# Performance work log

Hardware: AMD Instinct MI355X
Metric: run time of the kernel (lower is better)

## Reference

```python
import jax, jax.numpy as jnp
import numpy as np

NUM_HEADS = 8
WINDOW = 3
LOCAL_LEN = WINDOW * WINDOW
SR_RATIO = 8


def _normalize(v, eps=1e-12):
    n = jnp.linalg.norm(v, axis=-1, keepdims=True)
    return v / jnp.maximum(n, eps)


def _layernorm(v, g, b, eps=1e-5):
    m = v.mean(-1, keepdims=True)
    var = ((v - m) ** 2).mean(-1, keepdims=True)
    return (v - m) / jnp.sqrt(var + eps) * g + b


def _unfold3(x, H, W):
    # x: [B, C, H, W] -> [B, C, 9, H*W]  (kernel 3, pad 1, stride 1; torch nn.Unfold layout)
    B, C = x.shape[0], x.shape[1]
    xp = jnp.pad(x, ((0, 0), (0, 0), (1, 1), (1, 1)))
    patches = jnp.stack([xp[:, :, di:di + H, dj:dj + W]
                         for di in range(WINDOW) for dj in range(WINDOW)], axis=2)
    return patches.reshape(B, C, LOCAL_LEN, H * W)


def _forward(x, relative_coords_table, seq_length_scale, q_w, q_b, kv_w, kv_b,
             temperature, query_embedding, sr_w, sr_b, norm_g, norm_b,
             cpb_fc1_w, cpb_fc1_b, cpb_fc2_w, cpb_fc2_b,
             rel_bias_local, learnable_tokens, learnable_bias,
             proj_w, proj_b, relative_pos_index, padding_mask, H, W):
    B, N, C = x.shape
    hd = C // NUM_HEADS
    pool_H, pool_W = H // SR_RATIO, W // SR_RATIO
    pool_len = pool_H * pool_W

    # ---- queries ----
    q = (x @ q_w.T + q_b).reshape(B, N, NUM_HEADS, hd).transpose(0, 2, 1, 3)  # [B,h,N,d]
    q_norm = _normalize(q)
    q_scaled = (q_norm + query_embedding) * jax.nn.softplus(temperature) * seq_length_scale

    # ---- local k/v via unfold ----
    kv = x @ kv_w.T + kv_b  # [B,N,2C]
    k_loc = _normalize(kv[..., :C].reshape(B, N, NUM_HEADS, hd)).reshape(B, N, C)
    kv_img = jnp.concatenate([k_loc, kv[..., C:]], -1).transpose(0, 2, 1).reshape(B, 2 * C, H, W)
    kv_unf = _unfold3(kv_img, H, W).reshape(B, 2 * NUM_HEADS, hd, LOCAL_LEN, N)
    kv_unf = kv_unf.transpose(0, 1, 4, 2, 3)  # [B,2h,N,d,9]
    k_local, v_local = kv_unf[:, :NUM_HEADS], kv_unf[:, NUM_HEADS:]

    attn_local = jnp.einsum('bhnd,bhndl->bhnl', q_scaled, k_local) + rel_bias_local[:, None, :]
    attn_local = jnp.where(padding_mask, -jnp.inf, attn_local)

    # ---- pooled global k/v ----
    x_img = x.transpose(0, 2, 1).reshape(B, C, H, W)
    x_sr = jax.nn.gelu(jnp.einsum('oc,bchw->bohw', sr_w, x_img) + sr_b[None, :, None, None],
                       approximate=False)
    x_pool = x_sr.reshape(B, C, pool_H, SR_RATIO, pool_W, SR_RATIO).mean((3, 5))
    x_pool = x_pool.reshape(B, C, pool_len).transpose(0, 2, 1)
    x_pool = _layernorm(x_pool, norm_g, norm_b)
    kv_p = (x_pool @ kv_w.T + kv_b).reshape(B, pool_len, 2 * NUM_HEADS, hd).transpose(0, 2, 1, 3)
    k_pool, v_pool = kv_p[:, :NUM_HEADS], kv_p[:, NUM_HEADS:]

    # ---- continuous relative position bias (extrapolation path) ----
    cpb = jax.nn.relu(relative_coords_table @ cpb_fc1_w.T + cpb_fc1_b) @ cpb_fc2_w.T + cpb_fc2_b  # [T,h]
    pool_bias = cpb[relative_pos_index].reshape(N, pool_len, NUM_HEADS).transpose(2, 0, 1)  # [h,N,P]

    attn_pool = jnp.einsum('bhnd,bhpd->bhnp', q_scaled, _normalize(k_pool)) + pool_bias

    attn = jax.nn.softmax(jnp.concatenate([attn_local, attn_pool], -1), axis=-1)
    a_loc, a_pool = attn[..., :LOCAL_LEN], attn[..., LOCAL_LEN:]

    lt = jnp.einsum('bhnd,hdl->bhnl', q_norm, learnable_tokens) + learnable_bias + a_loc
    x_local = jnp.einsum('bhnl,bhndl->bhnd', lt, v_local)
    x_p = jnp.einsum('bhnp,bhpd->bhnd', a_pool, v_pool)
    out = (x_local + x_p).transpose(0, 2, 1, 3).reshape(B, N, C)
    return out @ proj_w.T + proj_b


def setup_inputs() -> dict:
    key = jax.random.key(0)
    B, H, W, C = 4, 64, 64, 256
    N = H * W
    hd = C // NUM_HEADS
    pool_H, pool_W = H // SR_RATIO, W // SR_RATIO
    pool_len = pool_H * pool_W

    # padding mask + per-query valid window length (get_seqlen_and_mask)
    ii, jj = np.meshgrid(np.arange(H), np.arange(W), indexing='ij')
    cols = []
    for di in range(WINDOW):
        for dj in range(WINDOW):
            ni, nj = ii + di - 1, jj + dj - 1
            cols.append(((ni < 0) | (ni >= H) | (nj < 0) | (nj >= W)).reshape(-1))
    padding_mask = np.stack(cols, -1)  # [N, 9], True = outside image
    local_len = (~padding_mask).sum(-1, keepdims=True).astype(np.float32)
    seq_length_scale = np.log(local_len + pool_len)  # [N, 1]

    # get_relative_position_cpb((H,W), (pool_H,pool_W))
    axis_q = np.arange(H, dtype=np.float64)
    axis_k = axis_q.reshape(pool_H, SR_RATIO).mean(-1)
    kh, kw = np.meshgrid(axis_k, axis_k, indexing='ij')
    qh, qw = np.meshgrid(axis_q, axis_q, indexing='ij')
    rel_h = (qh.ravel()[:, None] - kh.ravel()[None, :]) / (H - 1) * 8
    rel_w = (qw.ravel()[:, None] - kw.ravel()[None, :]) / (W - 1) * 8
    rel = np.stack([rel_h, rel_w], -1).reshape(-1, 2)
    table, idx = np.unique(rel, axis=0, return_inverse=True)
    table = np.sign(table) * np.log2(np.abs(table) + 1.0) / np.log2(8.0)

    ks = jax.random.split(key, 12)

    def nrm(k, shape, std=0.02):
        return jax.random.normal(k, shape, jnp.float32) * std

    return {
        'x': jax.random.normal(ks[0], (B, N, C), jnp.float32),
        'relative_coords_table': jnp.asarray(table, jnp.float32),
        'seq_length_scale': jnp.asarray(seq_length_scale, jnp.float32),
        'q_w': nrm(ks[1], (C, C)), 'q_b': jnp.zeros((C,), jnp.float32),
        'kv_w': nrm(ks[2], (2 * C, C)), 'kv_b': jnp.zeros((2 * C,), jnp.float32),
        'temperature': jnp.full((NUM_HEADS, 1, 1), float(np.log(np.expm1(1.0 / 0.24))), jnp.float32),
        'query_embedding': nrm(ks[3], (NUM_HEADS, 1, hd)),
        'sr_w': nrm(ks[4], (C, C)), 'sr_b': jnp.zeros((C,), jnp.float32),
        'norm_g': jnp.ones((C,), jnp.float32), 'norm_b': jnp.zeros((C,), jnp.float32),
        'cpb_fc1_w': nrm(ks[5], (512, 2), 0.1), 'cpb_fc1_b': jnp.zeros((512,), jnp.float32),
        'cpb_fc2_w': nrm(ks[6], (NUM_HEADS, 512)), 'cpb_fc2_b': jnp.zeros((NUM_HEADS,), jnp.float32),
        'rel_bias_local': nrm(ks[7], (NUM_HEADS, LOCAL_LEN), 0.0004),
        'learnable_tokens': nrm(ks[8], (NUM_HEADS, hd, LOCAL_LEN)),
        'learnable_bias': jnp.zeros((NUM_HEADS, 1, LOCAL_LEN), jnp.float32),
        'proj_w': nrm(ks[9], (C, C)), 'proj_b': jnp.zeros((C,), jnp.float32),
        'relative_pos_index': jnp.asarray(idx, jnp.int32),
        'padding_mask': jnp.asarray(padding_mask),
        'H': H, 'W': W,
    }


def reference(x, relative_coords_table, seq_length_scale, q_w, q_b, kv_w, kv_b,
              temperature, query_embedding, sr_w, sr_b, norm_g, norm_b,
              cpb_fc1_w, cpb_fc1_b, cpb_fc2_w, cpb_fc2_b,
              rel_bias_local, learnable_tokens, learnable_bias,
              proj_w, proj_b, relative_pos_index, padding_mask, H, W):
    return _forward(x, relative_coords_table, seq_length_scale, q_w, q_b, kv_w, kv_b,
                    temperature, query_embedding, sr_w, sr_b, norm_g, norm_b,
                    cpb_fc1_w, cpb_fc1_b, cpb_fc2_w, cpb_fc2_b,
                    rel_bias_local, learnable_tokens, learnable_bias,
                    proj_w, proj_b, relative_pos_index, padding_mask, H, W)
```

## Files before the change

kernel.cpp:

```cpp
#include <hip/hip_runtime.h>
#include <math.h>


typedef unsigned short ushort_t;
typedef __attribute__((ext_vector_type(8))) _Float16 half8;
typedef __attribute__((ext_vector_type(2))) _Float16 half2_t;
typedef __attribute__((ext_vector_type(4))) float f32x4;

static __device__ __forceinline__ ushort_t f2h(float f) {
    _Float16 h = (_Float16)f;
    return *(ushort_t*)&h;
}

static __device__ __forceinline__ float fdot2f(half2_t a, half2_t b, float c) {
#if __has_builtin(__builtin_amdgcn_fdot2)
    return __builtin_amdgcn_fdot2(a, b, c, false);
#else
    return (float)a[0] * (float)b[0] + (float)a[1] * (float)b[1] + c;
#endif
}

template <int CTRL>
static __device__ __forceinline__ float dpp_addf(float x) {
    int v = __builtin_amdgcn_update_dpp(
        0, __builtin_bit_cast(int, x), CTRL, 0xF, 0xF, true);
    return x + __builtin_bit_cast(float, v);
}
static __device__ __forceinline__ float quad_sumf(float x) {
    return dpp_addf<0x4E>(dpp_addf<0xB1>(x));
}
static __device__ __forceinline__ float sum16f(float x) {
    return dpp_addf<0x128>(dpp_addf<0x124>(quad_sumf(x)));
}

#define GLOAD16(g, l)                                                        \
    __builtin_amdgcn_global_load_lds(                                        \
        (const __attribute__((address_space(1))) unsigned int*)(g),          \
        (__attribute__((address_space(3))) unsigned int*)(l), 16, 0, 0)

template <int TM, int TN>
__global__ __launch_bounds__(256) void mfma_hgemm(
    const ushort_t* __restrict__ Ag, const ushort_t* __restrict__ Bg,
    const float* __restrict__ bias, float* __restrict__ out0,
    ushort_t* __restrict__ qh_out, ushort_t* __restrict__ kvh,
    ushort_t* __restrict__ xsrh, int mode)
{
    const int K = 256;
    const int IM = TM / 32;
    const int JN = TN / 32;
    __shared__ ushort_t Ah[2][TM * 32];
    __shared__ ushort_t Bh[2][TN * 32];

    const int t = threadIdx.x;
    const int w = t >> 6;
    const int lane = t & 63;
    const int bm = blockIdx.y * TM;
    const int bn = blockIdx.x * TN;
    const int wm = (w >> 1) * (TM / 2);
    const int wn = (w & 1) * (TN / 2);

    f32x4 acc[IM][JN];
#pragma unroll
    for (int i = 0; i < IM; ++i)
#pragma unroll
        for (int j = 0; j < JN; ++j) acc[i][j] = f32x4{0.f, 0.f, 0.f, 0.f};

    const int lrow  = t >> 2;
    const int lk8sw = ((t & 3) ^ ((t >> 3) & 3)) * 8;

#define STAGE(bufi, k0s)                                                     \
    do {                                                                     \
        _Pragma("unroll")                                                    \
        for (int r = 0; r < TM / 64; ++r)                                    \
            GLOAD16(Ag + (size_t)(bm + r * 64 + lrow) * K + (k0s) + lk8sw,   \
                    &Ah[bufi][(unsigned)(r * 64 + w * 16) * 32]);            \
        _Pragma("unroll")                                                    \
        for (int r = 0; r < TN / 64; ++r)                                    \
            GLOAD16(Bg + (size_t)(bn + r * 64 + lrow) * K + (k0s) + lk8sw,   \
                    &Bh[bufi][(unsigned)(r * 64 + w * 16) * 32]);            \
    } while (0)

    const int fr   = lane & 15;
    const int sws8 = ((lane >> 4) ^ ((fr >> 1) & 3)) * 8;

    STAGE(0, 0);
    __syncthreads();
    int buf = 0;
    for (int k0 = 0; k0 < K; k0 += 32) {
        if (k0 + 32 < K) STAGE(buf ^ 1, k0 + 32);

        half8 af[IM], bf[JN];
#pragma unroll
        for (int i = 0; i < IM; ++i)
            af[i] = *(const half8*)&Ah[buf][(unsigned)(wm + i * 16 + fr) * 32 + sws8];
#pragma unroll
        for (int j = 0; j < JN; ++j)
            bf[j] = *(const half8*)&Bh[buf][(unsigned)(wn + j * 16 + fr) * 32 + sws8];
#pragma unroll
        for (int i = 0; i < IM; ++i)
#pragma unroll
            for (int j = 0; j < JN; ++j)
                acc[i][j] = __builtin_amdgcn_mfma_f32_16x16x32_f16(af[i], bf[j], acc[i][j], 0, 0, 0);

        __syncthreads();
        buf ^= 1;
    }
#undef STAGE

    const int q4 = (lane >> 4) * 4;
#pragma unroll
    for (int i = 0; i < IM; ++i) {
#pragma unroll
        for (int jp = 0; jp < JN / 2; ++jp) {
#pragma unroll
            for (int r = 0; r < 4; ++r) {
                const int row = bm + wm + i * 16 + q4 + r;
                const int col0 = bn + wn + jp * 32 + fr;
                const int col1 = col0 + 16;
                float v0 = acc[i][2 * jp][r] + bias[col0];
                float v1 = acc[i][2 * jp + 1][r] + bias[col1];
                if (mode == 0) {
                    if (col0 < 256) {
                        qh_out[(size_t)row * 256 + col0] = f2h(v0);
                        qh_out[(size_t)row * 256 + col1] = f2h(v1);
                    } else if (col0 < 512) {
                        const float ss = sum16f(v0 * v0 + v1 * v1);
                        const float invn = 1.0f / fmaxf(sqrtf(ss), 1e-12f);
                        kvh[(size_t)row * 512 + (col0 - 256)] = f2h(v0 * invn);
                        kvh[(size_t)row * 512 + (col1 - 256)] = f2h(v1 * invn);
                    } else if (col0 < 768) {
                        kvh[(size_t)row * 512 + (col0 - 256)] = f2h(v0);
                        kvh[(size_t)row * 512 + (col1 - 256)] = f2h(v1);
                    } else {
                        v0 = 0.5f * v0 * (1.0f + erff(v0 * 0.70710678118654752f));
                        v1 = 0.5f * v1 * (1.0f + erff(v1 * 0.70710678118654752f));
                        xsrh[(size_t)row * 256 + (col0 - 768)] = f2h(v0);
                        xsrh[(size_t)row * 256 + (col1 - 768)] = f2h(v1);
                    }
                } else if (mode == 2) {
                    if (col0 < 256) {
                        const float ss = sum16f(v0 * v0 + v1 * v1);
                        const float invn = 1.0f / fmaxf(sqrtf(ss), 1e-12f);
                        v0 *= invn; v1 *= invn;
                    }
                    kvh[(size_t)row * 512 + col0] = f2h(v0);
                    kvh[(size_t)row * 512 + col1] = f2h(v1);
                } else {
                    out0[(size_t)row * 256 + col0] = v0;
                    out0[(size_t)row * 256 + col1] = v1;
                }
            }
        }
    }
}

__global__ __launch_bounds__(256) void prep_cpb(
    const float4* __restrict__ x, ushort4* __restrict__ xh, int n4, int nprep,
    const float* __restrict__ qw, const float* __restrict__ kvw,
    const float* __restrict__ srw, const float* __restrict__ pw,
    const float* __restrict__ qb, const float* __restrict__ kvb,
    const float* __restrict__ srb,
    ushort_t* __restrict__ Wall, ushort_t* __restrict__ Pw,
    float* __restrict__ ball,
    const float* __restrict__ table, const float* __restrict__ w1,
    const float* __restrict__ b1, const float* __restrict__ w2,
    const float* __restrict__ b2, float* __restrict__ outc, int T)
{
    if (blockIdx.x >= nprep) {
        const int wv = threadIdx.x >> 6;
        const int lane = threadIdx.x & 63;
        const int row = (blockIdx.x - nprep) * 4 + wv;
        if (row >= T) return;
        const float t0 = table[(size_t)row * 2];
        const float t1 = table[(size_t)row * 2 + 1];
        const int base = lane * 8;

        const float4* w1p = (const float4*)(w1 + (size_t)base * 2);
        float4 wa = w1p[0], wb = w1p[1], wc = w1p[2], wd = w1p[3];
        float4 ba = *(const float4*)(b1 + base);
        float4 bb = *(const float4*)(b1 + base + 4);
        float h[8];
        h[0] = fmaxf(fmaf(t1, wa.y, fmaf(t0, wa.x, ba.x)), 0.f);
        h[1] = fmaxf(fmaf(t1, wa.w, fmaf(t0, wa.z, ba.y)), 0.f);
        h[2] = fmaxf(fmaf(t1, wb.y, fmaf(t0, wb.x, ba.z)), 0.f);
        h[3] = fmaxf(fmaf(t1, wb.w, fmaf(t0, wb.z, ba.w)), 0.f);
        h[4] = fmaxf(fmaf(t1, wc.y, fmaf(t0, wc.x, bb.x)), 0.f);
        h[5] = fmaxf(fmaf(t1, wc.w, fmaf(t0, wc.z, bb.y)), 0.f);
        h[6] = fmaxf(fmaf(t1, wd.y, fmaf(t0, wd.x, bb.z)), 0.f);
        h[7] = fmaxf(fmaf(t1, wd.w, fmaf(t0, wd.z, bb.w)), 0.f);

#pragma unroll
        for (int hh = 0; hh < 8; ++hh) {
            const float4* w2p = (const float4*)(w2 + (size_t)hh * 512 + base);
            float4 p0 = w2p[0], p1 = w2p[1];
            float s = h[0]*p0.x + h[1]*p0.y + h[2]*p0.z + h[3]*p0.w
                    + h[4]*p1.x + h[5]*p1.y + h[6]*p1.z + h[7]*p1.w;
#pragma unroll
            for (int off = 1; off <= 32; off <<= 1) s += __shfl_xor(s, off);
            if (lane == 0) outc[(size_t)row * 8 + hh] = s + b2[hh];
        }
        return;
    }

    int idx = blockIdx.x * 256 + threadIdx.x;
    if (idx < n4) {
        float4 v = x[idx];
        ushort4 h;
        h.x = f2h(v.x); h.y = f2h(v.y); h.z = f2h(v.z); h.w = f2h(v.w);
        xh[idx] = h;
    }
    if (idx < 262144) {
        int nn = idx >> 8, k = idx & 255;
        float a;
        if (nn < 256)      a = qw[nn * 256 + k];
        else if (nn < 768) a = kvw[(nn - 256) * 256 + k];
        else               a = srw[(nn - 768) * 256 + k];
        Wall[idx] = f2h(a);
    }
    if (idx < 65536) Pw[idx] = f2h(pw[idx]);
    if (idx < 1024) {
        float bv;
        if (idx < 256)      bv = qb[idx];
        else if (idx < 768) bv = kvb[idx - 256];
        else                bv = srb[idx - 768];
        ball[idx] = bv;
    }
}

__global__ __launch_bounds__(256) void pool_ln(
    const ushort_t* __restrict__ xsr, const float* __restrict__ g,
    const float* __restrict__ be, ushort_t* __restrict__ xpool, int Hh, int Ww)
{
    const int C = 256;
    const int Nn = Hh * Ww;
    int b = blockIdx.x >> 6;
    int pidx = blockIdx.x & 63;
    int ph = pidx >> 3, pw = pidx & 7;
    int tid = threadIdx.x;
    float s = 0.f;
    for (int si = 0; si < 8; ++si) {
        int i = ph * 8 + si;
        const ushort_t* rowp = xsr + ((size_t)b * Nn + (size_t)i * Ww + pw * 8) * C + tid;
#pragma unroll
        for (int sj = 0; sj < 8; ++sj)
            s += (float)(*(const _Float16*)&rowp[(size_t)sj * C]);
    }
    s *= (1.f / 64.f);
    __shared__ float red[256];
    red[tid] = s; __syncthreads();
    for (int st = 128; st; st >>= 1) { if (tid < st) red[tid] += red[tid + st]; __syncthreads(); }
    float mean = red[0] * (1.f / 256.f);
    __syncthreads();
    float dv = s - mean;
    red[tid] = dv * dv; __syncthreads();
    for (int st = 128; st; st >>= 1) { if (tid < st) red[tid] += red[tid + st]; __syncthreads(); }
    float var = red[0] * (1.f / 256.f);
    xpool[(size_t)blockIdx.x * C + tid] = f2h(dv * rsqrtf(var + 1e-5f) * g[tid] + be[tid]);
}

__global__ __launch_bounds__(256) void attn_v8(
    const ushort_t* __restrict__ qh_g,
    const ushort_t* __restrict__ kvh,
    const ushort_t* __restrict__ kvph,
    const int* __restrict__ rpi,
    const float* __restrict__ cpbB,
    const float* __restrict__ sls, const float* __restrict__ temp,
    const float* __restrict__ qe, const float* __restrict__ rbl,
    const float* __restrict__ ltok, const float* __restrict__ lbias,
    ushort_t* __restrict__ attno_hf)
{
    const int h = blockIdx.y, b = blockIdx.z;
    const int t = threadIdx.x;
    const int i = blockIdx.x;

    __shared__ half8 kp_s[64][4];
    __shared__ half8 vp_s[64][4];
    __shared__ ushort_t pb_s[64][66];
    __shared__ float lts[9][32];
    __shared__ float rbl_s[9], lb_s[9], qe_s[32];

    {
        const int p = t >> 2;
        const int g4s = t & 3;
        const ushort_t* gk = kvph + ((size_t)(b * 64 + p)) * 512 + h * 32 + g4s * 8;
        kp_s[p][g4s] = *(const half8*)gk;
        vp_s[p][g4s] = *(const half8*)(gk + 256);
        const int rbase = i * 4096;
        for (int u = t; u < 4096; u += 256) {
            const int idx = rpi[rbase + u];
            pb_s[u >> 6][u & 63] = f2h(cpbB[(size_t)idx * 8 + h]);
        }
        for (int u = t; u < 288; u += 256) lts[u % 9][u / 9] = ltok[h * 288 + u];
        if (t < 9)  { rbl_s[t] = rbl[h * 9 + t]; lb_s[t] = lbias[h * 9 + t]; }
        if (t >= 64 && t < 96) qe_s[t - 64] = qe[h * 32 + (t - 64)];
    }
    __syncthreads();

    const int w = t >> 6;
    const int lane = t & 63;
    const int qi = lane >> 2;
    const int g4 = lane & 3;
    const int co = g4 * 8;
    const int j = w * 16 + qi;
    const int n = i * 64 + j;
    const size_t gq = (size_t)b * 4096 + n;

    const float tm = temp[h];
    const float sp = (tm > 20.f) ? tm : log1pf(expf(tm));

    float qv[8];
    {
        const half8 q8 = *(const half8*)(qh_g + gq * 256 + h * 32 + co);
        float ss = 0.f;
#pragma unroll
        for (int d = 0; d < 8; ++d) { qv[d] = (float)q8[d]; ss += qv[d] * qv[d]; }
        ss = quad_sumf(ss);
        const float invn = 1.0f / fmaxf(sqrtf(ss), 1e-12f);
#pragma unroll
        for (int d = 0; d < 8; ++d) qv[d] *= invn;
    }

    float lt[9];
#pragma unroll
    for (int l = 0; l < 9; ++l) {
        float dl = 0.f;
        const float4* lw = (const float4*)&lts[l][co];
#pragma unroll
        for (int c4 = 0; c4 < 2; ++c4) {
            float4 w4 = lw[c4];
            dl += qv[4*c4+0]*w4.x + qv[4*c4+1]*w4.y + qv[4*c4+2]*w4.z + qv[4*c4+3]*w4.w;
        }
        dl = quad_sumf(dl);
        lt[l] = dl + lb_s[l];
    }

    const float scal = sp * sls[n];
    half2_t qh[4];
#pragma unroll
    for (int c = 0; c < 4; ++c) {
        float a = (qv[2*c+0] + qe_s[co + 2*c+0]) * scal;
        float bq = (qv[2*c+1] + qe_s[co + 2*c+1]) * scal;
        qh[c] = half2_t{(_Float16)a, (_Float16)bq};
    }

    float sl[9];
#pragma unroll
    for (int l = 0; l < 9; ++l) {
        const int di = l / 3 - 1, dj = l % 3 - 1;
        const int ii = i + di;
        const int jn = j + dj;
        const bool ok = (ii >= 0) && (ii < 64) && (jn >= 0) && (jn < 64);
        const int ic = max(min(ii, 63), 0);
        const int jc = max(min(jn, 63), 0);
        const half8 k8 = *(const half8*)(kvh + ((size_t)(b * 4096 + ic * 64 + jc)) * 512 + h * 32 + co);
        float dk = 0.f;
        dk = fdot2f(qh[0], __builtin_shufflevector(k8, k8, 0, 1), dk);
        dk = fdot2f(qh[1], __builtin_shufflevector(k8, k8, 2, 3), dk);
        dk = fdot2f(qh[2], __builtin_shufflevector(k8, k8, 4, 5), dk);
        dk = fdot2f(qh[3], __builtin_shufflevector(k8, k8, 6, 7), dk);
        dk = quad_sumf(dk);
        sl[l] = ok ? (dk + rbl_s[l]) : -INFINITY;
    }

    float m = sl[0];
#pragma unroll
    for (int l = 1; l < 9; ++l) m = fmaxf(m, sl[l]);

    half2_t oh[4];
#pragma unroll
    for (int c = 0; c < 4; ++c) oh[c] = half2_t{(_Float16)0.f, (_Float16)0.f};
    float Z = 0.f;

    for (int cch = 0; cch < 8; ++cch) {
        float s8[8];
        float pbv[8];
#pragma unroll
        for (int c = 0; c < 4; ++c) {
            const half2_t p2 = *(const half2_t*)&pb_s[j][cch * 8 + 2 * c];
            pbv[2*c]   = (float)p2[0];
            pbv[2*c+1] = (float)p2[1];
        }
#pragma unroll
        for (int k = 0; k < 8; ++k) {
            const int p = cch * 8 + k;
            const half8 k8 = kp_s[p][g4];
            float acc = 0.f;
            acc = fdot2f(qh[0], __builtin_shufflevector(k8, k8, 0, 1), acc);
            acc = fdot2f(qh[1], __builtin_shufflevector(k8, k8, 2, 3), acc);
            acc = fdot2f(qh[2], __builtin_shufflevector(k8, k8, 4, 5), acc);
            acc = fdot2f(qh[3], __builtin_shufflevector(k8, k8, 6, 7), acc);
            acc = quad_sumf(acc);
            s8[k] = acc + pbv[k];
        }
        float cmax = s8[0];
#pragma unroll
        for (int k = 1; k < 8; ++k) cmax = fmaxf(cmax, s8[k]);
        const float m_new = fmaxf(m, cmax);
        const float factor = __expf(m - m_new);
        Z *= factor;
        const _Float16 fh = (_Float16)factor;
        const half2_t f2 = half2_t{fh, fh};
#pragma unroll
        for (int c = 0; c < 4; ++c) oh[c] *= f2;
        m = m_new;
#pragma unroll
        for (int k = 0; k < 8; ++k) {
            const float a = __expf(s8[k] - m);
            Z += a;
            const _Float16 ah = (_Float16)a;
            const half2_t a2 = half2_t{ah, ah};
            const half8 v8 = vp_s[cch * 8 + k][g4];
            oh[0] = a2 * __builtin_shufflevector(v8, v8, 0, 1) + oh[0];
            oh[1] = a2 * __builtin_shufflevector(v8, v8, 2, 3) + oh[1];
            oh[2] = a2 * __builtin_shufflevector(v8, v8, 4, 5) + oh[2];
            oh[3] = a2 * __builtin_shufflevector(v8, v8, 6, 7) + oh[3];
        }
    }

#pragma unroll
    for (int l = 0; l < 9; ++l) { sl[l] = __expf(sl[l] - m); Z += sl[l]; }

#pragma unroll
    for (int l = 0; l < 9; ++l) {
        const int di = l / 3 - 1, dj = l % 3 - 1;
        const int ii = i + di;
        const int jn = j + dj;
        const bool ok = (ii >= 0) && (ii < 64) && (jn >= 0) && (jn < 64);
        const int ic = max(min(ii, 63), 0);
        const int jc = max(min(jn, 63), 0);
        const float coef = ok ? (sl[l] + lt[l] * Z) : 0.f;
        const half8 v8 = *(const half8*)(kvh + ((size_t)(b * 4096 + ic * 64 + jc)) * 512 + 256 + h * 32 + co);
        const _Float16 ch = (_Float16)coef;
        const half2_t c2 = half2_t{ch, ch};
        oh[0] = c2 * __builtin_shufflevector(v8, v8, 0, 1) + oh[0];
        oh[1] = c2 * __builtin_shufflevector(v8, v8, 2, 3) + oh[1];
        oh[2] = c2 * __builtin_shufflevector(v8, v8, 4, 5) + oh[2];
        oh[3] = c2 * __builtin_shufflevector(v8, v8, 6, 7) + oh[3];
    }

    const float invZ = 1.0f / Z;
    ushort4* outp = (ushort4*)(attno_hf + gq * 256 + h * 32 + co);
#pragma unroll
    for (int c4 = 0; c4 < 2; ++c4) {
        ushort4 u;
        u.x = f2h((float)oh[2*c4+0][0] * invZ);
        u.y = f2h((float)oh[2*c4+0][1] * invZ);
        u.z = f2h((float)oh[2*c4+1][0] * invZ);
        u.w = f2h((float)oh[2*c4+1][1] * invZ);
        outp[c4] = u;
    }
}

extern "C" void kernel_launch(void* const* d_in, const int* in_sizes, int n_in,
                              void* d_out, int out_size, void* d_ws, size_t ws_size,
                              hipStream_t stream)
{
    const float* x    = (const float*)d_in[0];
    const float* tbl  = (const float*)d_in[1];
    const float* sls  = (const float*)d_in[2];
    const float* q_w  = (const float*)d_in[3];
    const float* q_b  = (const float*)d_in[4];
    const float* kv_w = (const float*)d_in[5];
    const float* kv_b = (const float*)d_in[6];
    const float* temp = (const float*)d_in[7];
    const float* qe   = (const float*)d_in[8];
    const float* sr_w = (const float*)d_in[9];
    const float* sr_b = (const float*)d_in[10];
    const float* ng   = (const float*)d_in[11];
    const float* nb   = (const float*)d_in[12];
    const float* f1w  = (const float*)d_in[13];
    const float* f1b  = (const float*)d_in[14];
    const float* f2w  = (const float*)d_in[15];
    const float* f2b  = (const float*)d_in[16];
    const float* rbl  = (const float*)d_in[17];
    const float* ltok = (const float*)d_in[18];
    const float* lbias= (const float*)d_in[19];
    const float* pw   = (const float*)d_in[20];
    const float* pb   = (const float*)d_in[21];
    const int*   rpi  = (const int*)d_in[22];

    const int C = 256, Hh = 64, Ww = 64, Nn = Hh * Ww;
    const int B = in_sizes[0] / (Nn * C);
    const int T = in_sizes[1] / 2;
    const int M = B * Nn;

    float* ws = (float*)d_ws;
    size_t o = 0;
    ushort_t* qh    = (ushort_t*)(ws + o); o += (size_t)M * C / 2;
    ushort_t* kvh   = (ushort_t*)(ws + o); o += (size_t)M * C;
    ushort_t* xsrh  = (ushort_t*)(ws + o); o += (size_t)M * C / 2;
    ushort_t* xpoolh= (ushort_t*)(ws + o); o += (size_t)B * 64 * C / 2;
    ushort_t* kvph  = (ushort_t*)(ws + o); o += (size_t)B * 64 * C;
    float* cpbB  = ws + o; o += (size_t)T * 8;
    ushort_t* xh   = (ushort_t*)(ws + o); o += (size_t)M * C / 2;
    ushort_t* Wall = (ushort_t*)(ws + o); o += 1024 * 256 / 2;
    ushort_t* Pwh  = (ushort_t*)(ws + o); o += 256 * 256 / 2;
    float* ball = ws + o; o += 1024;
    ushort_t* attno_hf = xh;

    dim3 blk(256);
    const int n4x = M * C / 4;
    const int nprep = (n4x + 255) / 256;
    const int ncpb  = (T + 3) / 4;

    prep_cpb<<<nprep + ncpb, blk, 0, stream>>>(
        (const float4*)x, (ushort4*)xh, n4x,
        nprep, q_w, kv_w, sr_w, pw, q_b, kv_b, sr_b, Wall, Pwh, ball,
        tbl, f1w, f1b, f2w, f2b, cpbB, T);
    mfma_hgemm<128, 128><<<dim3(8, M / 128), blk, 0, stream>>>(
        xh, Wall, ball, nullptr, qh, kvh, xsrh, 0);
    pool_ln<<<B * 64, blk, 0, stream>>>(xsrh, ng, nb, xpoolh, Hh, Ww);
    mfma_hgemm<64, 64><<<dim3(8, (B * 64) / 64), blk, 0, stream>>>(
        xpoolh, Wall + 256 * 256, ball + 256, nullptr, nullptr, kvph, nullptr, 2);
    attn_v8<<<dim3(64, 8, B), blk, 0, stream>>>(
        qh, kvh, kvph, rpi, cpbB, sls, temp, qe, rbl, ltok, lbias, attno_hf);
    mfma_hgemm<64, 64><<<dim3(4, M / 64), blk, 0, stream>>>(
        attno_hf, Pwh, pb, (float*)d_out, nullptr, nullptr, nullptr, 1);
}
```

Measured before the change: 229.1 us.

## Pipeline GEMM loads with vmcnt waits, XCD-aware block remap, and narrower tiles

Restructures the fp16 MFMA GEMM main loop so that two stages are prefetched up front. Each step waits on a partial vmcnt count and a raw s_barrier instead of a full __syncthreads, letting global-to-LDS loads overlap compute. It raises wave priority around the MFMA block and remaps workgroup IDs so consecutive tiles land on the same XCD for L2 locality. The input projection GEMM switches to 128x64 tiles with twice as many blocks. The risks are subtle ordering hazards in the manual waitcnt/barrier scheme and a remap that assumes the block count is a multiple of 8.

After: 208.0 us. 9.2% less time.

```diff
diff --git a/kernel.cpp b/kernel.cpp
--- a/kernel.cpp
+++ b/kernel.cpp
@@ -48,14 +48,20 @@
     const int K = 256;
     const int IM = TM / 32;
     const int JN = TN / 32;
+    constexpr int LPS = TM / 64 + TN / 64;
     __shared__ ushort_t Ah[2][TM * 32];
     __shared__ ushort_t Bh[2][TN * 32];
 
     const int t = threadIdx.x;
     const int w = t >> 6;
     const int lane = t & 63;
-    const int bm = blockIdx.y * TM;
-    const int bn = blockIdx.x * TN;
+
+    const int nwg = gridDim.x * gridDim.y;
+    int wg = blockIdx.y * gridDim.x + blockIdx.x;
+    wg = (wg & 7) * (nwg >> 3) + (wg >> 3);
+    const int bm = (wg / gridDim.x) * TM;
+    const int bn = (wg % gridDim.x) * TN;
+
     const int wm = (w >> 1) * (TM / 2);
     const int wn = (w & 1) * (TN / 2);
 
@@ -83,28 +89,45 @@
     const int fr   = lane & 15;
     const int sws8 = ((lane >> 4) ^ ((fr >> 1) & 3)) * 8;
 
+#define COMPUTE(bufi)                                                        \
+    do {                                                                     \
+        half8 af[IM], bf[JN];                                                \
+        _Pragma("unroll")                                                    \
+        for (int i2 = 0; i2 < IM; ++i2)                                      \
+            af[i2] = *(const half8*)&Ah[bufi][(unsigned)(wm + i2 * 16 + fr) * 32 + sws8]; \
+        _Pragma("unroll")                                                    \
+        for (int j2 = 0; j2 < JN; ++j2)                                      \
+            bf[j2] = *(const half8*)&Bh[bufi][(unsigned)(wn + j2 * 16 + fr) * 32 + sws8]; \
+        __builtin_amdgcn_s_setprio(1);                                       \
+        _Pragma("unroll")                                                    \
+        for (int i2 = 0; i2 < IM; ++i2)                                      \
+            _Pragma("unroll")                                                \
+            for (int j2 = 0; j2 < JN; ++j2)                                  \
+                acc[i2][j2] = __builtin_amdgcn_mfma_f32_16x16x32_f16(        \
+                    af[i2], bf[j2], acc[i2][j2], 0, 0, 0);                   \
+        __builtin_amdgcn_s_setprio(0);                                       \
+    } while (0)
+
     STAGE(0, 0);
-    __syncthreads();
+    STAGE(1, 32);
     int buf = 0;
-    for (int k0 = 0; k0 < K; k0 += 32) {
-        if (k0 + 32 < K) STAGE(buf ^ 1, k0 + 32);
-
-        half8 af[IM], bf[JN];
-#pragma unroll
-        for (int i = 0; i < IM; ++i)
-            af[i] = *(const half8*)&Ah[buf][(unsigned)(wm + i * 16 + fr) * 32 + sws8];
-#pragma unroll
-        for (int j = 0; j < JN; ++j)
-            bf[j] = *(const half8*)&Bh[buf][(unsigned)(wn + j * 16 + fr) * 32 + sws8];
-#pragma unroll
-        for (int i = 0; i < IM; ++i)
-#pragma unroll
-            for (int j = 0; j < JN; ++j)
-                acc[i][j] = __builtin_amdgcn_mfma_f32_16x16x32_f16(af[i], bf[j], acc[i][j], 0, 0, 0);
-
-        __syncthreads();
+#pragma unroll
+    for (int s = 0; s < K / 32 - 1; ++s) {
+        asm volatile("s_waitcnt vmcnt(%0)" :: "n"(LPS) : "memory");
+        __builtin_amdgcn_s_barrier();
+        asm volatile("" ::: "memory");
+        COMPUTE(buf);
+        asm volatile("" ::: "memory");
+        __builtin_amdgcn_s_barrier();
+        asm volatile("" ::: "memory");
+        if (s + 2 < K / 32) STAGE(buf, (s + 2) * 32);
         buf ^= 1;
     }
+    asm volatile("s_waitcnt vmcnt(0)" ::: "memory");
+    __builtin_amdgcn_s_barrier();
+    asm volatile("" ::: "memory");
+    COMPUTE(buf);
+#undef COMPUTE
 #undef STAGE
 
     const int q4 = (lane >> 4) * 4;
@@ -507,7 +530,7 @@
         (const float4*)x, (ushort4*)xh, n4x,
         nprep, q_w, kv_w, sr_w, pw, q_b, kv_b, sr_b, Wall, Pwh, ball,
         tbl, f1w, f1b, f2w, f2b, cpbB, T);
-    mfma_hgemm<128, 128><<<dim3(8, M / 128), blk, 0, stream>>>(
+    mfma_hgemm<128, 64><<<dim3(16, M / 128), blk, 0, stream>>>(
         xh, Wall, ball, nullptr, qh, kvh, xsrh, 0);
     pool_ln<<<B * 64, blk, 0, stream>>>(xsrh, ng, nb, xpoolh, Hh, Ww);
     mfma_hgemm<64, 64><<<dim3(8, (B * 64) / 64), blk, 0, stream>>>(
```
